# Kernel tuning notes

Hardware: AMD Instinct MI355X
Metric: run time of the kernel (lower is better)

The kernel has to match this reference:

```python
import jax, jax.numpy as jnp
import numpy as np

B, S, D, H, L = 2, 4096, 768, 12, 4
DFF, WIN, MAXPOS = 3072, 256, 4098
DH = D // H
W1 = WIN // 2            # one-sided window = 128
NC = S // W1             # number of query chunks = 32
EPS = 1e-12              # LongformerConfig default layer_norm_eps
SCALE = 1.0 / float(np.sqrt(DH))


def _ln(x, g, b):
    m = x.mean(-1, keepdims=True)
    v = ((x - m) ** 2).mean(-1, keepdims=True)
    return (x - m) / jnp.sqrt(v + EPS) * g + b


def _fwd(inputs, lengths, pos_emb, tok_emb, ln_emb_g, ln_emb_b,
         Wq, bq, Wk, bk, Wv, bv, Wo, bo, ln1_g, ln1_b,
         Wi, bi, Wf, bf, ln2_g, ln2_b):
    # embeddings: roberta-style position ids start at padding_idx+1 = 2
    x = inputs + pos_emb[2:2 + S][None] + tok_emb[0][None, None]
    x = _ln(x, ln_emb_g, ln_emb_b)

    mask = jnp.arange(S)[None, :] < lengths[:, None]            # [B,S] valid tokens
    idx = jnp.arange(NC)[:, None] * W1 + jnp.arange(3 * W1)     # [NC,3W] into padded keys
    jglob = idx - W1                                            # global key positions
    key_valid = (jglob >= 0)[None] & (jglob[None] < lengths[:, None, None])  # [B,NC,3W]
    qpos = jnp.arange(W1)[:, None]
    kpos = jnp.arange(3 * W1)[None, :]
    band = (kpos >= qpos) & (kpos <= qpos + 2 * W1)             # [W,3W] sliding band
    valid = band[None, None, None] & key_valid[:, None, :, None, :]  # [B,1,NC,W,3W]
    qmask = mask.reshape(B, NC, W1).astype(inputs.dtype)

    for l in range(L):
        q = (x @ Wq[l] + bq[l]).reshape(B, S, H, DH) * SCALE
        k = (x @ Wk[l] + bk[l]).reshape(B, S, H, DH)
        v = (x @ Wv[l] + bv[l]).reshape(B, S, H, DH)
        kp = jnp.pad(k, ((0, 0), (W1, W1), (0, 0), (0, 0)))
        vp = jnp.pad(v, ((0, 0), (W1, W1), (0, 0), (0, 0)))
        kc = jnp.take(kp, idx, axis=1)                          # [B,NC,3W,H,DH]
        vc = jnp.take(vp, idx, axis=1)
        qc = q.reshape(B, NC, W1, H, DH)
        scores = jnp.einsum('bcqhd,bckhd->bhcqk', qc, kc)       # [B,H,NC,W,3W]
        scores = jnp.where(valid, scores, -1e9)
        probs = jax.nn.softmax(scores, axis=-1)
        probs = probs * qmask[:, None, :, :, None]              # zero padded query rows (HF behavior)
        ctx = jnp.einsum('bhcqk,bckhd->bcqhd', probs, vc).reshape(B, S, D)
        x = _ln(x + ctx @ Wo[l] + bo[l], ln1_g[l], ln1_b[l])
        h = jax.nn.gelu(x @ Wi[l] + bi[l], approximate=False)
        x = _ln(x + h @ Wf[l] + bf[l], ln2_g[l], ln2_b[l])
    return x


def setup_inputs() -> dict:
    ks = jax.random.split(jax.random.key(0), 16)
    s = jnp.float32(0.02)
    f = jax.random.normal
    return {
        'inputs': f(ks[0], (B, S, D), jnp.float32),
        'lengths': jax.random.randint(ks[1], (B,), S // 2, S + 1),
        'pos_emb': s * f(ks[2], (MAXPOS, D), jnp.float32),
        'tok_emb': s * f(ks[3], (1, D), jnp.float32),
        'ln_emb_g': jnp.ones((D,), jnp.float32), 'ln_emb_b': jnp.zeros((D,), jnp.float32),
        'Wq': s * f(ks[4], (L, D, D), jnp.float32), 'bq': jnp.zeros((L, D), jnp.float32),
        'Wk': s * f(ks[5], (L, D, D), jnp.float32), 'bk': jnp.zeros((L, D), jnp.float32),
        'Wv': s * f(ks[6], (L, D, D), jnp.float32), 'bv': jnp.zeros((L, D), jnp.float32),
        'Wo': s * f(ks[7], (L, D, D), jnp.float32), 'bo': jnp.zeros((L, D), jnp.float32),
        'ln1_g': jnp.ones((L, D), jnp.float32), 'ln1_b': jnp.zeros((L, D), jnp.float32),
        'Wi': s * f(ks[8], (L, D, DFF), jnp.float32), 'bi': jnp.zeros((L, DFF), jnp.float32),
        'Wf': s * f(ks[9], (L, DFF, D), jnp.float32), 'bf': jnp.zeros((L, D), jnp.float32),
        'ln2_g': jnp.ones((L, D), jnp.float32), 'ln2_b': jnp.zeros((L, D), jnp.float32),
    }


def reference(inputs, lengths, pos_emb, tok_emb, ln_emb_g, ln_emb_b,
              Wq, bq, Wk, bk, Wv, bv, Wo, bo, ln1_g, ln1_b,
              Wi, bi, Wf, bf, ln2_g, ln2_b):
    return _fwd(inputs, lengths, pos_emb, tok_emb, ln_emb_g, ln_emb_b,
                Wq, bq, Wk, bk, Wv, bv, Wo, bo, ln1_g, ln1_b,
                Wi, bi, Wf, bf, ln2_g, ln2_b)
```

## Files before the change

kernel.cpp:

```cpp
#include <hip/hip_runtime.h>
#include <cstdint>

#define S_LEN 4096
#define D_MODEL 768
#define NHEAD 12
#define DHE 64
#define DFF_ 3072
#define NL 4
#define W1_ 128
#define NC_ 32
#define QKVN 2304

typedef __attribute__((ext_vector_type(8))) short v8s;
typedef __attribute__((ext_vector_type(4))) short v4s;
typedef __attribute__((ext_vector_type(4))) float v4f;

__device__ __forceinline__ short f2bf(float f) {
  union { float f; unsigned u; } x; x.f = f;
  unsigned r = x.u + 0x7fffu + ((x.u >> 16) & 1u);
  return (short)(r >> 16);
}

__device__ __forceinline__ float b2f(short s) {
  union { unsigned u; float f; } x; x.u = ((unsigned)(unsigned short)s) << 16;
  return x.f;
}

__device__ __forceinline__ void load_lds16(const short* g, short* l) {
  __builtin_amdgcn_global_load_lds((const __attribute__((address_space(1))) void*)g,
                                   (__attribute__((address_space(3))) void*)l, 16, 0, 0);
}

template<int NB, int EPI, int WRV>
__global__ __launch_bounds__(512, 4)
void gemm128(const short* __restrict__ A, const short* __restrict__ Bt,
             const float* __restrict__ bias, void* __restrict__ outp,
             short* __restrict__ vtw, int M, int N, int K)
{
  constexpr int CF = NB / 64;
  constexpr int BI = NB / 64;
  constexpr int SI = 2 + BI;
  __shared__ short sA[2][128 * 64];
  __shared__ short sB[2][NB * 64];
  const int tid = threadIdx.x;
  const int lane = tid & 63, wid = tid >> 6;
  const int g = lane >> 4, l16 = lane & 15;
  const int wr = wid >> 2, wc = wid & 3;
  const int nt = K >> 6;

  const int gx = gridDim.x;
  const int nwg = gx * gridDim.y;
  const int p = blockIdx.y * gx + blockIdx.x;
  const int q8 = nwg >> 3;
  const int lb = (p & 7) * q8 + (p >> 3);
  const int bn_ = lb % gx, bm_ = lb / gx;

  const short* Ab = A + (size_t)(bm_ * 128) * K;
  const short* Bb = Bt + (size_t)(bn_ * NB) * K;

  auto stage = [&](int t, int bufi) {
#pragma unroll
    for (int i = 0; i < 2; ++i) {
      const int byte = i * 8192 + tid * 16;
      const int row = byte >> 7;
      const int lir = (byte & 127) ^ ((row & 7) << 4);
      load_lds16(Ab + (size_t)row * K + t * 64 + (lir >> 1),
                 &sA[bufi][(i * 8192 + wid * 1024) >> 1]);
    }
#pragma unroll
    for (int i = 0; i < BI; ++i) {
      const int byte = i * 8192 + tid * 16;
      const int row = byte >> 7;
      const int lir = (byte & 127) ^ ((row & 7) << 4);
      load_lds16(Bb + (size_t)row * K + t * 64 + (lir >> 1),
                 &sB[bufi][(i * 8192 + wid * 1024) >> 1]);
    }
  };

  auto ldf = [&](const short* plane, int row, int kk) -> v8s {
    const int b = (kk * 64 + g * 16) ^ ((row & 7) << 4);
    return *(const v8s*)((const char*)plane + row * 128 + b);
  };

  v4f acc[4][CF] = {};

  stage(0, 0);
  stage(1, 1);
  asm volatile("s_waitcnt vmcnt(%0)" :: "i"(SI) : "memory");
  __builtin_amdgcn_s_barrier();

  for (int t = 0; t < nt; ++t) {
    const int cur = t & 1;
    const short* pA = sA[cur];
    const short* pB = sB[cur];
    v8s fa[2][4], fb[2][CF];
#pragma unroll
    for (int kk = 0; kk < 2; ++kk) {
#pragma unroll
      for (int m = 0; m < 4; ++m) fa[kk][m] = ldf(pA, wr * 64 + m * 16 + l16, kk);
#pragma unroll
      for (int n = 0; n < CF; ++n) fb[kk][n] = ldf(pB, wc * (CF * 16) + n * 16 + l16, kk);
    }
    asm volatile("s_waitcnt lgkmcnt(0)" ::: "memory");
    __builtin_amdgcn_sched_barrier(0);
    __builtin_amdgcn_s_barrier();
    if (t + 2 < nt) stage(t + 2, cur);
    __builtin_amdgcn_sched_barrier(0);
    __builtin_amdgcn_s_setprio(1);
#pragma unroll
    for (int kk = 0; kk < 2; ++kk)
#pragma unroll
      for (int m = 0; m < 4; ++m)
#pragma unroll
        for (int n = 0; n < CF; ++n)
          acc[m][n] = __builtin_amdgcn_mfma_f32_16x16x32_bf16(fa[kk][m], fb[kk][n], acc[m][n], 0, 0, 0);
    __builtin_amdgcn_s_setprio(0);
    __builtin_amdgcn_sched_barrier(0);
    if (t + 2 < nt) {
      asm volatile("s_waitcnt vmcnt(%0)" :: "i"(SI) : "memory");
    } else if (t + 1 < nt) {
      asm volatile("s_waitcnt vmcnt(0)" ::: "memory");
    }
    if (t + 1 < nt) __builtin_amdgcn_s_barrier();
  }

  const int row0 = bm_ * 128 + wr * 64;
  const int col0 = bn_ * NB + wc * (CF * 16);
#pragma unroll
  for (int m = 0; m < 4; ++m)
#pragma unroll
    for (int n = 0; n < CF; ++n) {
      const int col = col0 + n * 16 + l16;
      const float bc = bias[col];
      short pk4[4];
#pragma unroll
      for (int r = 0; r < 4; ++r) {
        const int row = row0 + m * 16 + g * 4 + r;
        const float v = acc[m][n][r] + bc;
        short o;
        if (EPI == 2) {
          const float e = __expf(1.5957691216057308f * (v + 0.044715f * v * v * v));
          o = f2bf(v - v / (1.0f + e));
        } else {
          o = f2bf(v);
        }
        ((short*)outp)[(size_t)row * N + col] = o;
        pk4[r] = o;
      }
      if (WRV) {
        if (col0 >= 1536) {
          const int cc = col - 1536;
          const int h = cc >> 6, d = cc & 63;
          const int rowm = row0 + m * 16 + g * 4;
          const int b = rowm >> 12, s = rowm & (S_LEN - 1);
          v4s pk = { pk4[0], pk4[1], pk4[2], pk4[3] };
          *(v4s*)&vtw[(((size_t)b * NHEAD + h) * DHE + d) * S_LEN + s] = pk;
        }
      }
    }
}

__global__ __launch_bounds__(256)
void transpose_w(const float* __restrict__ in, short* __restrict__ out, int K, int N,
                 size_t in_ls, size_t out_ls, float scale)
{
  __shared__ float t[32][33];
  const int n0 = blockIdx.x * 32, k0 = blockIdx.y * 32;
  const float* src = in + (size_t)blockIdx.z * in_ls;
  short* dst = out + (size_t)blockIdx.z * out_ls;
  const int tx = threadIdx.x, ty = threadIdx.y;
#pragma unroll
  for (int i = 0; i < 4; ++i)
    t[ty + 8*i][tx] = src[(size_t)(k0 + ty + 8*i) * N + n0 + tx];
  __syncthreads();
#pragma unroll
  for (int i = 0; i < 4; ++i)
    dst[(size_t)(n0 + ty + 8*i) * K + k0 + tx] = f2bf(t[tx][ty + 8*i] * scale);
}

__global__ void prep_bias(const float* __restrict__ bq, const float* __restrict__ bk,
                          const float* __restrict__ bv, float* __restrict__ out)
{
  const int l = blockIdx.x, p = blockIdx.y, c = threadIdx.x;
  const float* s = p == 0 ? bq : (p == 1 ? bk : bv);
  out[(l * 3 + p) * 768 + c] = s[l * 768 + c] * (p == 0 ? 0.125f : 1.0f);
}

template<int MODE, int FINAL>
__global__ __launch_bounds__(256)
void ln_kernel(const void* __restrict__ in0, const void* __restrict__ in1,
               const float* __restrict__ in2,
               const float* __restrict__ gamma, const float* __restrict__ beta,
               float* __restrict__ outf, short* __restrict__ outb)
{
  __shared__ float red[8];
  const int row = blockIdx.x;
  const int tid = threadIdx.x;
  const int wave = tid >> 6, lane = tid & 63;
  float v[3];
#pragma unroll
  for (int i = 0; i < 3; ++i) {
    const int c = tid + i * 256;
    const size_t idx = (size_t)row * D_MODEL + c;
    if (MODE == 0) {
      const int s = row & (S_LEN - 1);
      v[i] = ((const float*)in0)[idx] + ((const float*)in1)[(size_t)(2 + s) * D_MODEL + c] + in2[c];
    } else {
      v[i] = b2f(((const short*)in0)[idx]) + b2f(((const short*)in1)[idx]);
    }
  }
  float sum = v[0] + v[1] + v[2];
#pragma unroll
  for (int m = 1; m < 64; m <<= 1) sum += __shfl_xor(sum, m, 64);
  if (lane == 0) red[wave] = sum;
  __syncthreads();
  const float mean = (red[0] + red[1] + red[2] + red[3]) * (1.0f / 768.0f);
  float sq = 0.f;
#pragma unroll
  for (int i = 0; i < 3; ++i) { float d = v[i] - mean; sq += d * d; }
#pragma unroll
  for (int m = 1; m < 64; m <<= 1) sq += __shfl_xor(sq, m, 64);
  if (lane == 0) red[4 + wave] = sq;
  __syncthreads();
  const float var = (red[4] + red[5] + red[6] + red[7]) * (1.0f / 768.0f);
  const float rstd = 1.0f / sqrtf(var + 1e-12f);
#pragma unroll
  for (int i = 0; i < 3; ++i) {
    const int c = tid + i * 256;
    const size_t idx = (size_t)row * D_MODEL + c;
    const float o = (v[i] - mean) * rstd * gamma[c] + beta[c];
    if (FINAL) outf[idx] = o;
    outb[idx] = f2bf(o);
  }
}

__global__ __launch_bounds__(256, 2)
void att_fused(const short* __restrict__ qkv, const short* __restrict__ vt,
               const int* __restrict__ lengths, short* __restrict__ ctx)
{
  __shared__ __align__(16) short KP[320 * 64];
  __shared__ __align__(16) short Vl[64 * 320];
  const int p = blockIdx.x;
  const int lb = (p & 7) * 192 + (p >> 3);
  const int hq = lb & 1, c = (lb >> 1) & 31, bh = lb >> 6;
  const int b = bh / 12, h = bh - b * 12;
  const int len = lengths[b];
  const int tid = threadIdx.x;
  const int wave = tid >> 6, lane = tid & 63;
  const int g = lane >> 4, l16 = lane & 15;
  const int j0h = c * W1_ + hq * 64 - W1_;

  {
    const int row0 = tid >> 3;
    const int o = (tid & 7) * 16;
    const char* kcol = (const char*)qkv + (size_t)b * S_LEN * 4608 + 1536 + h * 128;
#pragma unroll
    for (int i = 0; i < 10; ++i) {
      const int r_ = i * 32 + row0;
      const int op = o ^ ((r_ & 7) << 4);
      int jg = j0h + r_;
      jg = jg < 0 ? 0 : (jg > S_LEN - 1 ? S_LEN - 1 : jg);
      load_lds16((const short*)(kcol + (size_t)jg * 4608 + op),
                 (short*)((char*)KP + i * 4096 + wave * 1024));
    }
  }
  {
    const char* vrow = (const char*)vt + ((size_t)(b * NHEAD + h) * DHE) * (S_LEN * 2);
#pragma unroll
    for (int r = 0; r < 10; ++r) {
      const int off = r * 4096 + tid * 16;
      const int rw = (int)(((unsigned)off * 6554u) >> 22);
      const int o = off - rw * 640;
      int jb = j0h * 2 + (o ^ ((rw & 7) << 4));
      jb = jb < 0 ? 0 : (jb > S_LEN * 2 - 16 ? S_LEN * 2 - 16 : jb);
      load_lds16((const short*)(vrow + (size_t)rw * (S_LEN * 2) + jb),
                 (short*)((char*)Vl + r * 4096 + wave * 1024));
    }
  }
  const int qrow = c * W1_ + hq * 64 + wave * 16 + l16;
  const short* qp = qkv + (size_t)(b * S_LEN + qrow) * QKVN + h * DHE;
  const v8s a0 = *(const v8s*)(qp + g * 8);
  const v8s a1 = *(const v8s*)(qp + 32 + g * 8);

  asm volatile("s_waitcnt vmcnt(0)" ::: "memory");
  __builtin_amdgcn_sched_barrier(0);
  __builtin_amdgcn_s_barrier();

  v4f s[20];
  const int kswz = (l16 & 7) << 4;
#pragma unroll
  for (int nt = 0; nt < 20; ++nt) {
    const char* krow = (const char*)KP + (nt * 16 + l16) * 128;
    const v8s k0 = *(const v8s*)(krow + ((g * 16) ^ kswz));
    const v8s k1 = *(const v8s*)(krow + ((64 + g * 16) ^ kswz));
    v4f t = {0.f, 0.f, 0.f, 0.f};
    t = __builtin_amdgcn_mfma_f32_16x16x32_bf16(k0, a0, t, 0, 0, 0);
    t = __builtin_amdgcn_mfma_f32_16x16x32_bf16(k1, a1, t, 0, 0, 0);
    s[nt] = t;
  }

  const int qloc = wave * 16 + l16;
  float m = -3.0e38f;
#pragma unroll
  for (int nt = 0; nt < 20; ++nt)
#pragma unroll
    for (int r = 0; r < 4; ++r) {
      const int j = nt * 16 + g * 4 + r;
      const int jg = j0h + j;
      const bool ok = (j >= qloc) & (j <= qloc + 2 * W1_) & (jg >= 0) & (jg < len);
      const float v = ok ? s[nt][r] : -1e9f;
      s[nt][r] = v;
      m = fmaxf(m, v);
    }
  m = fmaxf(m, __shfl_xor(m, 16, 64));
  m = fmaxf(m, __shfl_xor(m, 32, 64));
  float su = 0.f;
#pragma unroll
  for (int nt = 0; nt < 20; ++nt)
#pragma unroll
    for (int r = 0; r < 4; ++r) {
      const float e = __expf(s[nt][r] - m);
      s[nt][r] = e;
      su += e;
    }
  su += __shfl_xor(su, 16, 64);
  su += __shfl_xor(su, 32, 64);
  const float f = (qrow < len) ? 1.0f / su : 0.0f;

  __builtin_amdgcn_s_barrier();
  const int pswz = (qloc & 7) << 4;
  char* prow = (char*)KP + qloc * 640;
#pragma unroll
  for (int nt = 0; nt < 20; ++nt) {
    v4s pk;
#pragma unroll
    for (int r = 0; r < 4; ++r) pk[r] = f2bf(s[nt][r] * f);
    *(v4s*)(prow + ((nt * 32 + g * 8) ^ pswz)) = pk;
  }
  asm volatile("s_waitcnt lgkmcnt(0)" ::: "memory");
  __builtin_amdgcn_sched_barrier(0);

  v4f acc[4] = {};
#pragma unroll
  for (int kc = 0; kc < 10; ++kc) {
    const v8s fa = *(const v8s*)(prow + ((kc * 64 + g * 16) ^ pswz));
#pragma unroll
    for (int dt = 0; dt < 4; ++dt) {
      const int vr = dt * 16 + l16;
      const v8s fb = *(const v8s*)((char*)Vl + vr * 640 + ((kc * 64 + g * 16) ^ ((vr & 7) << 4)));
      acc[dt] = __builtin_amdgcn_mfma_f32_16x16x32_bf16(fa, fb, acc[dt], 0, 0, 0);
    }
  }
  const int srow0 = c * W1_ + hq * 64 + wave * 16;
#pragma unroll
  for (int dt = 0; dt < 4; ++dt)
#pragma unroll
    for (int r = 0; r < 4; ++r)
      ctx[(size_t)(b * S_LEN + srow0 + g * 4 + r) * D_MODEL + h * DHE + dt * 16 + l16] = f2bf(acc[dt][r]);
}

extern "C" void kernel_launch(void* const* d_in, const int* in_sizes, int n_in,
                              void* d_out, int out_size, void* d_ws, size_t ws_size,
                              hipStream_t stream) {
  (void)in_sizes; (void)n_in; (void)out_size; (void)ws_size;
  const float* inputs  = (const float*)d_in[0];
  const int*   lengths = (const int*)d_in[1];
  const float* pos_emb = (const float*)d_in[2];
  const float* tok_emb = (const float*)d_in[3];
  const float* ln_emb_g = (const float*)d_in[4];
  const float* ln_emb_b = (const float*)d_in[5];
  const float* Wq = (const float*)d_in[6];
  const float* bq = (const float*)d_in[7];
  const float* Wk = (const float*)d_in[8];
  const float* bk = (const float*)d_in[9];
  const float* Wv = (const float*)d_in[10];
  const float* bv = (const float*)d_in[11];
  const float* Wo = (const float*)d_in[12];
  const float* bo = (const float*)d_in[13];
  const float* ln1_g = (const float*)d_in[14];
  const float* ln1_b = (const float*)d_in[15];
  const float* Wi = (const float*)d_in[16];
  const float* bi = (const float*)d_in[17];
  const float* Wf = (const float*)d_in[18];
  const float* bf2 = (const float*)d_in[19];
  const float* ln2_g = (const float*)d_in[20];
  const float* ln2_b = (const float*)d_in[21];

  const size_t MTOK = (size_t)2 * S_LEN;
  const size_t DD  = (size_t)D_MODEL * D_MODEL;
  const size_t DDF = (size_t)D_MODEL * DFF_;

  char* ws = (char*)d_ws;
  size_t off = 0;
  auto alloc = [&](size_t bytes) { void* p = ws + off; off += (bytes + 255) & ~(size_t)255; return p; };

  short* xb    = (short*)alloc(MTOK * D_MODEL * 2);
  short* qkv   = (short*)alloc(MTOK * QKVN * 2);
  short* vtb   = (short*)alloc(MTOK * D_MODEL * 2);
  short* yb    = (short*)alloc(MTOK * D_MODEL * 2);
  short* ctxb  = (short*)alloc(MTOK * D_MODEL * 2);
  short* hb    = (short*)alloc(MTOK * DFF_ * 2);
  short* wqkvt = (short*)alloc((size_t)NL * QKVN * D_MODEL * 2);
  short* wot   = (short*)alloc((size_t)NL * DD * 2);
  short* wit   = (short*)alloc((size_t)NL * DDF * 2);
  short* wft   = (short*)alloc((size_t)NL * DDF * 2);
  float* bqkv  = (float*)alloc((size_t)NL * QKVN * 4);
  float* x = (float*)d_out;

  const dim3 tb(32, 8);
  const size_t QL = (size_t)QKVN * D_MODEL;
  transpose_w<<<dim3(24, 24, NL), tb, 0, stream>>>(Wq, wqkvt,            D_MODEL, D_MODEL, DD, QL, 0.125f);
  transpose_w<<<dim3(24, 24, NL), tb, 0, stream>>>(Wk, wqkvt + 768*768,  D_MODEL, D_MODEL, DD, QL, 1.0f);
  transpose_w<<<dim3(24, 24, NL), tb, 0, stream>>>(Wv, wqkvt + 1536*768, D_MODEL, D_MODEL, DD, QL, 1.0f);
  transpose_w<<<dim3(24, 24, NL), tb, 0, stream>>>(Wo, wot, D_MODEL, D_MODEL, DD, DD, 1.0f);
  transpose_w<<<dim3(96, 24, NL), tb, 0, stream>>>(Wi, wit, D_MODEL, DFF_, DDF, DDF, 1.0f);
  transpose_w<<<dim3(24, 96, NL), tb, 0, stream>>>(Wf, wft, DFF_, D_MODEL, DDF, DDF, 1.0f);
  prep_bias<<<dim3(NL, 3), 768, 0, stream>>>(bq, bk, bv, bqkv);

  ln_kernel<0, 0><<<MTOK, 256, 0, stream>>>(inputs, pos_emb, tok_emb, ln_emb_g, ln_emb_b, x, xb);

  for (int l = 0; l < NL; ++l) {
    gemm128<128, 0, 1><<<dim3(18, 64), 512, 0, stream>>>(xb, wqkvt + (size_t)l * QL, bqkv + (size_t)l * QKVN,
                                                         qkv, vtb, (int)MTOK, QKVN, D_MODEL);
    att_fused<<<dim3(1536), 256, 0, stream>>>(qkv, vtb, lengths, ctxb);
    gemm128<64, 0, 0><<<dim3(12, 64), 512, 0, stream>>>(ctxb, wot + (size_t)l * DD, bo + l * D_MODEL,
                                                        yb, nullptr, (int)MTOK, D_MODEL, D_MODEL);
    ln_kernel<1, 0><<<MTOK, 256, 0, stream>>>(xb, yb, nullptr, ln1_g + l * D_MODEL, ln1_b + l * D_MODEL, x, xb);
    gemm128<128, 2, 0><<<dim3(24, 64), 512, 0, stream>>>(xb, wit + (size_t)l * DDF, bi + l * DFF_,
                                                         hb, nullptr, (int)MTOK, DFF_, D_MODEL);
    gemm128<64, 0, 0><<<dim3(12, 64), 512, 0, stream>>>(hb, wft + (size_t)l * DDF, bf2 + l * D_MODEL,
                                                        yb, nullptr, (int)MTOK, D_MODEL, DFF_);
    if (l < NL - 1)
      ln_kernel<1, 0><<<MTOK, 256, 0, stream>>>(xb, yb, nullptr, ln2_g + l * D_MODEL, ln2_b + l * D_MODEL, x, xb);
    else
      ln_kernel<1, 1><<<MTOK, 256, 0, stream>>>(xb, yb, nullptr, ln2_g + l * D_MODEL, ln2_b + l * D_MODEL, x, xb);
  }
}
```

Measured before the change: 876.0 us.

## Overlap V tile loads with QK scores and merge QKVO weight transposes

In the attention kernel the Q fragment loads now issue before the V tile loads, and the first wait only drains the K and Q loads (vmcnt(10)). This lets the ten V async copies stay in flight during the QK^T MFMAs and softmax, with a full wait placed just before the P·V phase. Separately, the four Q/K/V/O weight-transpose launches are merged into one kernel that selects source and destination from blockIdx.z, saving three launches. The partial wait relies on the exact count and order of outstanding memory ops, which the sched barriers are there to pin.

```diff
diff --git a/kernel.cpp b/kernel.cpp
--- a/kernel.cpp
+++ b/kernel.cpp
@@ -161,6 +161,30 @@
 }
 
 __global__ __launch_bounds__(256)
+void qkvo_trans(const float* __restrict__ Wq, const float* __restrict__ Wk,
+                const float* __restrict__ Wv, const float* __restrict__ Wo,
+                short* __restrict__ wqkvt, short* __restrict__ wot)
+{
+  __shared__ float t[32][33];
+  const int n0 = blockIdx.x * 32, k0 = blockIdx.y * 32;
+  const int l = blockIdx.z & 3, m = blockIdx.z >> 2;
+  const size_t DD = (size_t)D_MODEL * D_MODEL;
+  const size_t QL = (size_t)QKVN * D_MODEL;
+  const float* src = (m == 0 ? Wq : m == 1 ? Wk : m == 2 ? Wv : Wo) + (size_t)l * DD;
+  short* dst = (m < 3) ? (wqkvt + (size_t)l * QL + (size_t)m * D_MODEL * D_MODEL)
+                       : (wot + (size_t)l * DD);
+  const float scale = (m == 0) ? 0.125f : 1.0f;
+  const int tx = threadIdx.x, ty = threadIdx.y;
+#pragma unroll
+  for (int i = 0; i < 4; ++i)
+    t[ty + 8*i][tx] = src[(size_t)(k0 + ty + 8*i) * D_MODEL + n0 + tx];
+  __syncthreads();
+#pragma unroll
+  for (int i = 0; i < 4; ++i)
+    dst[(size_t)(n0 + ty + 8*i) * D_MODEL + k0 + tx] = f2bf(t[tx][ty + 8*i] * scale);
+}
+
+__global__ __launch_bounds__(256)
 void transpose_w(const float* __restrict__ in, short* __restrict__ out, int K, int N,
                  size_t in_ls, size_t out_ls, float scale)
 {
@@ -264,6 +288,12 @@
                  (short*)((char*)KP + i * 4096 + wave * 1024));
     }
   }
+  __builtin_amdgcn_sched_barrier(0);
+  const int qrow = c * W1_ + hq * 64 + wave * 16 + l16;
+  const short* qp = qkv + (size_t)(b * S_LEN + qrow) * QKVN + h * DHE;
+  const v8s a0 = *(const v8s*)(qp + g * 8);
+  const v8s a1 = *(const v8s*)(qp + 32 + g * 8);
+  __builtin_amdgcn_sched_barrier(0);
   {
     const char* vrow = (const char*)vt + ((size_t)(b * NHEAD + h) * DHE) * (S_LEN * 2);
 #pragma unroll
@@ -277,12 +307,8 @@
                  (short*)((char*)Vl + r * 4096 + wave * 1024));
     }
   }
-  const int qrow = c * W1_ + hq * 64 + wave * 16 + l16;
-  const short* qp = qkv + (size_t)(b * S_LEN + qrow) * QKVN + h * DHE;
-  const v8s a0 = *(const v8s*)(qp + g * 8);
-  const v8s a1 = *(const v8s*)(qp + 32 + g * 8);
-
-  asm volatile("s_waitcnt vmcnt(0)" ::: "memory");
+  __builtin_amdgcn_sched_barrier(0);
+  asm volatile("s_waitcnt vmcnt(10)" ::: "memory");
   __builtin_amdgcn_sched_barrier(0);
   __builtin_amdgcn_s_barrier();
 
@@ -327,6 +353,8 @@
   su += __shfl_xor(su, 32, 64);
   const float f = (qrow < len) ? 1.0f / su : 0.0f;
 
+  asm volatile("s_waitcnt vmcnt(0)" ::: "memory");
+  __builtin_amdgcn_sched_barrier(0);
   __builtin_amdgcn_s_barrier();
   const int pswz = (qloc & 7) << 4;
   char* prow = (char*)KP + qloc * 640;
@@ -409,10 +437,7 @@
 
   const dim3 tb(32, 8);
   const size_t QL = (size_t)QKVN * D_MODEL;
-  transpose_w<<<dim3(24, 24, NL), tb, 0, stream>>>(Wq, wqkvt,            D_MODEL, D_MODEL, DD, QL, 0.125f);
-  transpose_w<<<dim3(24, 24, NL), tb, 0, stream>>>(Wk, wqkvt + 768*768,  D_MODEL, D_MODEL, DD, QL, 1.0f);
-  transpose_w<<<dim3(24, 24, NL), tb, 0, stream>>>(Wv, wqkvt + 1536*768, D_MODEL, D_MODEL, DD, QL, 1.0f);
-  transpose_w<<<dim3(24, 24, NL), tb, 0, stream>>>(Wo, wot, D_MODEL, D_MODEL, DD, DD, 1.0f);
+  qkvo_trans<<<dim3(24, 24, 16), tb, 0, stream>>>(Wq, Wk, Wv, Wo, wqkvt, wot);
   transpose_w<<<dim3(96, 24, NL), tb, 0, stream>>>(Wi, wit, D_MODEL, DFF_, DDF, DDF, 1.0f);
   transpose_w<<<dim3(24, 96, NL), tb, 0, stream>>>(Wf, wft, DFF_, D_MODEL, DDF, DDF, 1.0f);
   prep_bias<<<dim3(NL, 3), 768, 0, stream>>>(bq, bk, bv, bqkv);
```

Result: no change. 870.1 us (-0.7%).
